# Performance work log

Hardware: AMD Instinct MI355X
Metric: run time of the kernel (lower is better)

The kernel has to match this reference:

```python
import jax, jax.numpy as jnp
import numpy as np

E = 8        # num_experts
TOPK = 2     # k
D = 1024     # input/output size
H = 4096     # expert hidden size


def setup_inputs() -> dict:
    key = jax.random.key(0)
    ks = jax.random.split(key, 8)
    s = 0.02
    return {
        "hidden_states": jax.random.normal(ks[0], (2, 2048, D), dtype=jnp.float32),
        "Wr": jax.random.normal(ks[1], (D, E), dtype=jnp.float32) * s,
        "br": jnp.zeros((E,), dtype=jnp.float32),
        "gate_bias": jnp.zeros((E,), dtype=jnp.float32),
        "W1": jax.random.normal(ks[2], (E, D, H), dtype=jnp.float32) * s,
        "b1": jnp.zeros((E, H), dtype=jnp.float32),
        "W2": jax.random.normal(ks[3], (E, H, D), dtype=jnp.float32) * s,
        "b2": jnp.zeros((E, D), dtype=jnp.float32),
    }


def reference(hidden_states, Wr, br, gate_bias, W1, b1, W2, b2):
    B, S, Din = hidden_states.shape
    x = hidden_states.reshape(B * S, Din)              # [T, D]
    # Router: logits + gate bias, top-k, softmax over the k selected logits
    logits = x @ Wr + br + gate_bias                   # [T, E]
    top_v, top_i = jax.lax.top_k(logits, TOPK)         # [T, k]
    probs = jax.nn.softmax(top_v, axis=-1)             # [T, k]
    # Scatter top-k probs into dense per-expert gate weights [T, E]
    gate = jnp.einsum("tk,tke->te", probs,
                      jax.nn.one_hot(top_i, E, dtype=probs.dtype))
    # Per-expert MLP (exact gelu, eval mode -> no dropout/noise),
    # weighted-combine; zero gate weight == token not routed to expert.
    out = jnp.zeros((B * S, W2.shape[-1]), dtype=x.dtype)
    for e in range(E):
        h = jax.nn.gelu(x @ W1[e] + b1[e], approximate=False)  # [T, H]
        y = h @ W2[e] + b2[e]                                  # [T, D]
        out = out + gate[:, e:e + 1] * y
    return out.reshape(B, S, -1)
```

## Files before the change

kernel.cpp:

```cpp
#include <hip/hip_runtime.h>
#include <hip/hip_bf16.h>
#include <stdint.h>
#include <stddef.h>


#define T_TOK 4096
#define DIM   1024
#define HID   4096
#define NE    8
#define MT_MAX 40

typedef unsigned short u16;
typedef __bf16 bf16x8 __attribute__((ext_vector_type(8)));
typedef float  f32x4  __attribute__((ext_vector_type(4)));
typedef u16    u16x8  __attribute__((ext_vector_type(8)));

__device__ __forceinline__ u16 f2bf(float f) {
  union { float f; uint32_t u; } v; v.f = f;
  uint32_t u = v.u;
  return (u16)((u + 0x7fffu + ((u >> 16) & 1u)) >> 16);
}

__device__ __forceinline__ void async_load16(const void* g, void* l) {
  typedef __attribute__((address_space(1))) void GPtr;
  typedef __attribute__((address_space(3))) void LPtr;
  __builtin_amdgcn_global_load_lds((GPtr*)g, (LPtr*)l, 16, 0, 0);
}

__global__ void router_kernel(const float* __restrict__ x, const float* __restrict__ Wr,
                              const float* __restrict__ br, const float* __restrict__ gb,
                              int* __restrict__ counts, int* __restrict__ lists,
                              float* __restrict__ gate_p) {
  const int t = blockIdx.x * 4 + (threadIdx.x >> 6);
  const int lane = threadIdx.x & 63;
  const float* xr = x + (size_t)t * DIM;
  float acc[NE];
#pragma unroll
  for (int e = 0; e < NE; ++e) acc[e] = 0.f;
#pragma unroll
  for (int i = 0; i < DIM / 64; ++i) {
    const int k = i * 64 + lane;
    const float xv = xr[k];
    const float4 w0 = *reinterpret_cast<const float4*>(Wr + (size_t)k * NE);
    const float4 w1 = *reinterpret_cast<const float4*>(Wr + (size_t)k * NE + 4);
    acc[0] += xv * w0.x; acc[1] += xv * w0.y; acc[2] += xv * w0.z; acc[3] += xv * w0.w;
    acc[4] += xv * w1.x; acc[5] += xv * w1.y; acc[6] += xv * w1.z; acc[7] += xv * w1.w;
  }
#pragma unroll
  for (int off = 32; off >= 1; off >>= 1) {
#pragma unroll
    for (int e = 0; e < NE; ++e) acc[e] += __shfl_xor(acc[e], off);
  }
  if (lane == 0) {
    float lg[NE];
#pragma unroll
    for (int e = 0; e < NE; ++e) lg[e] = acc[e] + br[e] + gb[e];
    int i0 = 0;
#pragma unroll
    for (int e = 1; e < NE; ++e) if (lg[e] > lg[i0]) i0 = e;
    int i1 = (i0 == 0) ? 1 : 0;
#pragma unroll
    for (int e = 0; e < NE; ++e) if (e != i0 && lg[e] > lg[i1]) i1 = e;
    const float ev = expf(lg[i1] - lg[i0]);
    const float p0 = 1.f / (1.f + ev);
    const float p1 = ev / (1.f + ev);
    const int pos0 = atomicAdd(&counts[i0], 1);
    lists[i0 * T_TOK + pos0] = t * 2 + 0;
    const int pos1 = atomicAdd(&counts[i1], 1);
    lists[i1 * T_TOK + pos1] = t * 2 + 1;
    gate_p[t * 2 + 0] = p0;
    gate_p[t * 2 + 1] = p1;
  }
}

__global__ void tile_table_kernel(const int* __restrict__ counts, int* __restrict__ tab) {
  if (threadIdx.x == 0) {
    int tot = 0;
    for (int e = 0; e < NE; ++e) {
      const int c = counts[e];
      const int nt = (c + 255) >> 8;
      for (int i = 0; i < nt && tot < MT_MAX; ++i) {
        tab[tot * 2] = e; tab[tot * 2 + 1] = i * 256; ++tot;
      }
    }
    for (; tot < MT_MAX; ++tot) tab[tot * 2] = -1;
  }
}

__global__ void cvt_x_kernel(const float* __restrict__ in, u16* __restrict__ out) {
  const int i = blockIdx.x * blockDim.x + threadIdx.x;
  const int t = i >> 7;
  const int d0 = (i & 127) * 8;
  const float4 a = *reinterpret_cast<const float4*>(in + (size_t)t * DIM + d0);
  const float4 b = *reinterpret_cast<const float4*>(in + (size_t)t * DIM + d0 + 4);
  u16x8 r;
  r[0] = f2bf(a.x); r[1] = f2bf(a.y); r[2] = f2bf(a.z); r[3] = f2bf(a.w);
  r[4] = f2bf(b.x); r[5] = f2bf(b.y); r[6] = f2bf(b.z); r[7] = f2bf(b.w);
  *reinterpret_cast<u16x8*>(out + (size_t)(d0 >> 6) * (T_TOK * 64) +
                            (size_t)t * 64 + (d0 & 63)) = r;
}

__global__ void cvt_w_kernel(const float* __restrict__ in, u16* __restrict__ out,
                             int K, int N) {
  __shared__ float tile[64][65];
  const int e = blockIdx.z;
  const int n0 = blockIdx.x * 64, k0 = blockIdx.y * 64;
  const int tid = threadIdx.x;
  const float* src = in + (size_t)e * K * N;
#pragma unroll
  for (int r = 0; r < 16; ++r) {
    const int kr = r * 4 + (tid >> 6);
    tile[kr][tid & 63] = src[(size_t)(k0 + kr) * N + n0 + (tid & 63)];
  }
  __syncthreads();
  u16* dst = out + (size_t)e * K * N + (size_t)(k0 >> 6) * ((size_t)N * 64);
#pragma unroll
  for (int r = 0; r < 8; ++r) {
    const int nr = r * 8 + (tid >> 5);
    const int kc = (tid & 31) * 2;
    ushort2 v;
    v.x = f2bf(tile[kc][nr]);
    v.y = f2bf(tile[kc + 1][nr]);
    *reinterpret_cast<ushort2*>(&dst[(size_t)(n0 + nr) * 64 + kc]) = v;
  }
}

template <int KT, int NT, int NSPLIT, int PHASE>
__global__ __launch_bounds__(512, 2)
void gemm_kernel(const u16* __restrict__ Abase, const u16* __restrict__ Bt,
                 const float* __restrict__ bias, const int* __restrict__ counts,
                 const int* __restrict__ lists, const float* __restrict__ gate_p,
                 const int* __restrict__ tab,
                 u16* __restrict__ hout, float* __restrict__ yout) {
  const int e = tab[blockIdx.x * 2];
  if (e < 0) return;
  const int m0 = tab[blockIdx.x * 2 + 1];
  const int cnt = counts[e];
  const int n0 = blockIdx.y * 256;
  const int z = blockIdx.z;
  const int kb64 = z * ((KT / NSPLIT) / 64);
  constexpr int nkt = (KT / NSPLIT) / 64;
  constexpr int niter = nkt / 2;
  constexpr size_t AKT = (PHASE == 1) ? (size_t)T_TOK * 64 : (size_t)T_TOK * 2 * 64;
  constexpr size_t BKT = (size_t)NT * 64;
  constexpr size_t HSLAB = (size_t)T_TOK * 2 * 64;

  const int tid = threadIdx.x;
  const int lane = tid & 63, w = tid >> 6;
  const int wm = w >> 2, wn = w & 3;
  const int bh = wn >> 1, bs = wn & 1;
  const int l15 = lane & 15, lks = lane >> 4;

  __shared__ alignas(16) u16 lds[65536];
  __shared__ int rowp[256];

  if (tid < 256) {
    const int idx = m0 + tid;
    rowp[tid] = lists[e * T_TOK + (idx < cnt ? idx : cnt - 1)];
  }
  __syncthreads();

  const int sslot = (tid & 7) ^ ((tid >> 3) & 7);
  const u16* aPtr[2][2];
  const u16* bPtr[2][2];
#pragma unroll
  for (int h = 0; h < 2; ++h)
#pragma unroll
    for (int s = 0; s < 2; ++s) {
      const int r = h * 128 + s * 64 + (tid >> 3);
      const int p = rowp[r];
      const int arow = (PHASE == 1) ? (p >> 1) : p;
      aPtr[h][s] = Abase + (size_t)kb64 * AKT + (size_t)arow * 64 + sslot * 8;
      bPtr[h][s] = Bt + (size_t)e * NT * KT + (size_t)kb64 * BKT +
                   (size_t)(n0 + r) * 64 + sslot * 8;
    }

  int aoff[2];
#pragma unroll
  for (int k = 0; k < 2; ++k)
    aoff[k] = l15 * 64 + (((k * 4 + lks) ^ (l15 & 7)) * 8);

  f32x4 acc[8][4];
#pragma unroll
  for (int a = 0; a < 8; ++a)
#pragma unroll
    for (int b = 0; b < 4; ++b) acc[a][b] = f32x4{0.f, 0.f, 0.f, 0.f};

  bf16x8 af[4][2], bfr[4][2];

#define RDA(C, FMH)                                                            \
  _Pragma("unroll") for (int f_ = 0; f_ < 4; ++f_)                             \
  _Pragma("unroll") for (int k_ = 0; k_ < 2; ++k_)                             \
    af[f_][k_] = *reinterpret_cast<const bf16x8*>(                             \
        &lds[(((C) * 2 + wm) * 2 + (FMH)) * 4096 + f_ * 1024 + aoff[k_]]);

#define RDB(C)                                                                 \
  _Pragma("unroll") for (int g_ = 0; g_ < 4; ++g_)                             \
  _Pragma("unroll") for (int k_ = 0; k_ < 2; ++k_)                             \
    bfr[g_][k_] = *reinterpret_cast<const bf16x8*>(                            \
        &lds[32768 + (((C) * 2 + bh) * 2 + bs) * 4096 + g_ * 1024 + aoff[k_]]);

#define SGA(C, S, TT)                                                          \
  _Pragma("unroll") for (int h_ = 0; h_ < 2; ++h_)                             \
    async_load16(aPtr[h_][S] + (size_t)(TT) * AKT,                             \
                 &lds[(((C) * 2 + h_) * 2 + (S)) * 4096 + w * 512]);

#define SGB(C, H, TT)                                                          \
  _Pragma("unroll") for (int s_ = 0; s_ < 2; ++s_)                             \
    async_load16(bPtr[H][s_] + (size_t)(TT) * BKT,                             \
                 &lds[32768 + (((C) * 2 + (H)) * 2 + s_) * 4096 + w * 512]);

#define MMQ(FMH, FNH)                                                          \
  _Pragma("unroll") for (int f_ = 0; f_ < 4; ++f_)                             \
  _Pragma("unroll") for (int g_ = 0; g_ < 2; ++g_)                             \
  _Pragma("unroll") for (int k_ = 0; k_ < 2; ++k_)                             \
    acc[(FMH) * 4 + f_][(FNH) * 2 + g_] =                                      \
        __builtin_amdgcn_mfma_f32_16x16x32_bf16(                               \
            af[f_][k_], bfr[(FNH) * 2 + g_][k_],                               \
            acc[(FMH) * 4 + f_][(FNH) * 2 + g_], 0, 0, 0);

#define CORE(FMH, FNH)                                                         \
  __builtin_amdgcn_s_barrier();                                                \
  asm volatile("s_waitcnt lgkmcnt(0)" ::: "memory");                           \
  __builtin_amdgcn_sched_barrier(0);                                           \
  __builtin_amdgcn_s_setprio(1);                                               \
  MMQ(FMH, FNH);                                                               \
  __builtin_amdgcn_s_setprio(0);                                               \
  __builtin_amdgcn_sched_barrier(0);

#define BAR() __builtin_amdgcn_s_barrier();

#define ITER(T, LAST)                                                          \
  {                                                                            \
    RDA(0, 0); RDB(0);                                                         \
    SGA(1, 1, (T) + 1);                                                        \
    CORE(0, 0) BAR()                                                           \
    if (!(LAST)) { SGA(0, 0, (T) + 2); }                                       \
    CORE(0, 1) BAR()                                                           \
    RDA(0, 1);                                                                 \
    if (!(LAST)) { SGB(0, 0, (T) + 2); }                                       \
    CORE(1, 0) BAR()                                                           \
    if (!(LAST)) { SGB(0, 1, (T) + 2); }                                       \
    CORE(1, 1)                                                                 \
    if (LAST) { asm volatile("s_waitcnt vmcnt(0)" ::: "memory"); }             \
    else      { asm volatile("s_waitcnt vmcnt(6)" ::: "memory"); }             \
    __builtin_amdgcn_sched_barrier(0);                                         \
    BAR()                                                                      \
    RDA(1, 0); RDB(1);                                                         \
    if (!(LAST)) { SGA(0, 1, (T) + 2); }                                       \
    CORE(0, 0) BAR()                                                           \
    if (!(LAST)) { SGA(1, 0, (T) + 3); }                                       \
    CORE(0, 1) BAR()                                                           \
    RDA(1, 1);                                                                 \
    if (!(LAST)) { SGB(1, 0, (T) + 3); }                                       \
    CORE(1, 0) BAR()                                                           \
    if (!(LAST)) { SGB(1, 1, (T) + 3); }                                       \
    CORE(1, 1)                                                                 \
    if (!(LAST)) {                                                             \
      asm volatile("s_waitcnt vmcnt(6)" ::: "memory");                         \
      __builtin_amdgcn_sched_barrier(0);                                       \
    }                                                                          \
    BAR()                                                                      \
  }

  SGA(0, 0, 0); SGB(0, 0, 0); SGB(0, 1, 0); SGA(0, 1, 0);
  SGA(1, 0, 1); SGB(1, 0, 1); SGB(1, 1, 1);
  asm volatile("s_waitcnt vmcnt(6)" ::: "memory");
  __builtin_amdgcn_sched_barrier(0);
  __builtin_amdgcn_s_barrier();

  for (int it = 0; it < niter - 1; ++it) {
    const int t = 2 * it;
    ITER(t, false);
  }
  ITER(nkt - 2, true);

#undef ITER
#undef CORE
#undef MMQ
#undef SGB
#undef SGA
#undef RDB
#undef RDA
#undef BAR

  const float* bias_e = bias + (size_t)e * NT;
  const float bz = (z == 0) ? 1.f : 0.f;
#pragma unroll
  for (int fm = 0; fm < 8; ++fm) {
    const int rbase = wm * 128 + (fm >> 2) * 64 + (fm & 3) * 16 + (lane >> 4) * 4;
#pragma unroll
    for (int r = 0; r < 4; ++r) {
      const int row = rbase + r;
      if (m0 + row >= cnt) continue;
      const int p = rowp[row];
#pragma unroll
      for (int nf = 0; nf < 4; ++nf) {
        const int n = n0 + wn * 64 + nf * 16 + l15;
        const float v = acc[fm][nf][r];
        if (PHASE == 1) {
          const float vb = v + bias_e[n];
          const float g = 0.5f * vb * (1.0f + erff(vb * 0.70710678118654752f));
          hout[(size_t)(n >> 6) * HSLAB + (size_t)p * 64 + (n & 63)] = f2bf(g);
        } else if (PHASE == 2) {
          yout[(size_t)z * T_TOK * 2 * NT + (size_t)p * NT + n] =
              gate_p[p] * (v + bz * bias_e[n]);
        } else {
          atomicAdd(&yout[(size_t)(p >> 1) * NT + n], gate_p[p] * (v + bz * bias_e[n]));
        }
      }
    }
  }
}

__global__ void combine4_kernel(const float* __restrict__ yp, float* __restrict__ out) {
  const int i = blockIdx.x * blockDim.x + threadIdx.x;
  const int t = i >> 8, d4 = i & 255;
  const size_t r0 = (size_t)(2 * t) * 256 + d4;
  const size_t zoff = (size_t)T_TOK * 2 * DIM / 4;
  const float4 a = reinterpret_cast<const float4*>(yp)[r0];
  const float4 b = reinterpret_cast<const float4*>(yp)[r0 + 256];
  const float4 c = reinterpret_cast<const float4*>(yp)[zoff + r0];
  const float4 d = reinterpret_cast<const float4*>(yp)[zoff + r0 + 256];
  float4 o;
  o.x = a.x + b.x + c.x + d.x; o.y = a.y + b.y + c.y + d.y;
  o.z = a.z + b.z + c.z + d.z; o.w = a.w + b.w + c.w + d.w;
  reinterpret_cast<float4*>(out)[i] = o;
}

extern "C" void kernel_launch(void* const* d_in, const int* in_sizes, int n_in,
                              void* d_out, int out_size, void* d_ws, size_t ws_size,
                              hipStream_t stream) {
  const float* x  = (const float*)d_in[0];
  const float* Wr = (const float*)d_in[1];
  const float* br = (const float*)d_in[2];
  const float* gb = (const float*)d_in[3];
  const float* W1 = (const float*)d_in[4];
  const float* b1 = (const float*)d_in[5];
  const float* W2 = (const float*)d_in[6];
  const float* b2 = (const float*)d_in[7];
  float* out = (float*)d_out;

  char* ws = (char*)d_ws;
  size_t off = 0;
  int*   counts = (int*)(ws + off);   off += 256;
  int*   ttab   = (int*)(ws + off);   off += 512;
  int*   lists  = (int*)(ws + off);   off += (size_t)NE * T_TOK * 4;
  float* gate_p = (float*)(ws + off); off += (size_t)T_TOK * 2 * 4;
  u16*   xb     = (u16*)(ws + off);   off += (size_t)T_TOK * DIM * 2;
  u16*   wbuf   = (u16*)(ws + off);   off += (size_t)NE * DIM * HID * 2;
  u16*   hbuf   = (u16*)(ws + off);   off += (size_t)T_TOK * 2 * HID * 2;
  float* ypair  = (float*)(ws + off);
  const size_t need_full = off + (size_t)2 * T_TOK * 2 * DIM * 4;
  const bool use_ypair = (ws_size >= need_full);

  hipMemsetAsync(counts, 0, 32, stream);
  router_kernel<<<T_TOK / 4, 256, 0, stream>>>(x, Wr, br, gb, counts, lists, gate_p);
  tile_table_kernel<<<1, 64, 0, stream>>>(counts, ttab);
  cvt_x_kernel<<<T_TOK * DIM / 8 / 256, 256, 0, stream>>>(x, xb);
  cvt_w_kernel<<<dim3(HID / 64, DIM / 64, NE), 256, 0, stream>>>(W1, wbuf, DIM, HID);
  gemm_kernel<DIM, HID, 1, 1><<<dim3(MT_MAX, HID / 256, 1), 512, 0, stream>>>(
      xb, wbuf, b1, counts, lists, gate_p, ttab, hbuf, nullptr);
  cvt_w_kernel<<<dim3(DIM / 64, HID / 64, NE), 256, 0, stream>>>(W2, wbuf, HID, DIM);
  if (use_ypair) {
    gemm_kernel<HID, DIM, 2, 2><<<dim3(MT_MAX, DIM / 256, 2), 512, 0, stream>>>(
        hbuf, wbuf, b2, counts, lists, gate_p, ttab, nullptr, ypair);
    combine4_kernel<<<T_TOK * DIM / 4 / 256, 256, 0, stream>>>(ypair, out);
  } else {
    hipMemsetAsync(out, 0, (size_t)out_size * 4, stream);
    gemm_kernel<HID, DIM, 2, 3><<<dim3(MT_MAX, DIM / 256, 2), 512, 0, stream>>>(
        hbuf, wbuf, b2, counts, lists, gate_p, ttab, nullptr, out);
  }
}
```

Before: 508.0 us.

## Replace quarter-tile ping-pong schedule with simple double-buffered K loop

Replaces the interleaved schedule in the GEMM main loop with a plain double-buffered loop. The old schedule split each K-tile into quarters, each behind its own barrier, and kept loads two tiles ahead. Now each step issues all A/B async loads for the next 64-wide K slice into the other buffer, computes two half-tiles of MFMAs, then waits for all loads and takes a single barrier. The LDS layout is simplified to contiguous 256-row buffers. The intent is to cut barrier and synchronisation overhead, at the cost of a shorter prefetch distance and a full vmcnt(0) wait each step that may expose memory latency.

Measured after the change: 498.6 us. No clear change (-1.9%).

```diff
diff --git a/kernel.cpp b/kernel.cpp
--- a/kernel.cpp
+++ b/kernel.cpp
@@ -140,7 +140,6 @@
   const int z = blockIdx.z;
   const int kb64 = z * ((KT / NSPLIT) / 64);
   constexpr int nkt = (KT / NSPLIT) / 64;
-  constexpr int niter = nkt / 2;
   constexpr size_t AKT = (PHASE == 1) ? (size_t)T_TOK * 64 : (size_t)T_TOK * 2 * 64;
   constexpr size_t BKT = (size_t)NT * 64;
   constexpr size_t HSLAB = (size_t)T_TOK * 2 * 64;
@@ -148,7 +147,6 @@
   const int tid = threadIdx.x;
   const int lane = tid & 63, w = tid >> 6;
   const int wm = w >> 2, wn = w & 3;
-  const int bh = wn >> 1, bs = wn & 1;
   const int l15 = lane & 15, lks = lane >> 4;
 
   __shared__ alignas(16) u16 lds[65536];
@@ -161,19 +159,17 @@
   __syncthreads();
 
   const int sslot = (tid & 7) ^ ((tid >> 3) & 7);
-  const u16* aPtr[2][2];
-  const u16* bPtr[2][2];
-#pragma unroll
-  for (int h = 0; h < 2; ++h)
-#pragma unroll
-    for (int s = 0; s < 2; ++s) {
-      const int r = h * 128 + s * 64 + (tid >> 3);
-      const int p = rowp[r];
-      const int arow = (PHASE == 1) ? (p >> 1) : p;
-      aPtr[h][s] = Abase + (size_t)kb64 * AKT + (size_t)arow * 64 + sslot * 8;
-      bPtr[h][s] = Bt + (size_t)e * NT * KT + (size_t)kb64 * BKT +
-                   (size_t)(n0 + r) * 64 + sslot * 8;
-    }
+  const u16* aP[4];
+  const u16* bP[4];
+#pragma unroll
+  for (int i = 0; i < 4; ++i) {
+    const int r = i * 64 + (tid >> 3);
+    const int p = rowp[r];
+    const int arow = (PHASE == 1) ? (p >> 1) : p;
+    aP[i] = Abase + (size_t)kb64 * AKT + (size_t)arow * 64 + sslot * 8;
+    bP[i] = Bt + (size_t)e * NT * KT + (size_t)kb64 * BKT +
+            (size_t)(n0 + r) * 64 + sslot * 8;
+  }
 
   int aoff[2];
 #pragma unroll
@@ -187,102 +183,70 @@
     for (int b = 0; b < 4; ++b) acc[a][b] = f32x4{0.f, 0.f, 0.f, 0.f};
 
   bf16x8 af[4][2], bfr[4][2];
+
+#define SGALL(C, TT)                                                           \
+  _Pragma("unroll") for (int i_ = 0; i_ < 4; ++i_)                             \
+    async_load16(aP[i_] + (size_t)(TT) * AKT,                                  \
+                 &lds[(C) * 16384 + (i_ * 64 + w * 8) * 64]);                  \
+  _Pragma("unroll") for (int i_ = 0; i_ < 4; ++i_)                             \
+    async_load16(bP[i_] + (size_t)(TT) * BKT,                                  \
+                 &lds[32768 + (C) * 16384 + (i_ * 64 + w * 8) * 64]);
 
 #define RDA(C, FMH)                                                            \
   _Pragma("unroll") for (int f_ = 0; f_ < 4; ++f_)                             \
   _Pragma("unroll") for (int k_ = 0; k_ < 2; ++k_)                             \
     af[f_][k_] = *reinterpret_cast<const bf16x8*>(                             \
-        &lds[(((C) * 2 + wm) * 2 + (FMH)) * 4096 + f_ * 1024 + aoff[k_]]);
+        &lds[(C) * 16384 + (wm * 128 + (FMH) * 64 + f_ * 16) * 64 + aoff[k_]]);
 
 #define RDB(C)                                                                 \
   _Pragma("unroll") for (int g_ = 0; g_ < 4; ++g_)                             \
   _Pragma("unroll") for (int k_ = 0; k_ < 2; ++k_)                             \
     bfr[g_][k_] = *reinterpret_cast<const bf16x8*>(                            \
-        &lds[32768 + (((C) * 2 + bh) * 2 + bs) * 4096 + g_ * 1024 + aoff[k_]]);
-
-#define SGA(C, S, TT)                                                          \
-  _Pragma("unroll") for (int h_ = 0; h_ < 2; ++h_)                             \
-    async_load16(aPtr[h_][S] + (size_t)(TT) * AKT,                             \
-                 &lds[(((C) * 2 + h_) * 2 + (S)) * 4096 + w * 512]);
-
-#define SGB(C, H, TT)                                                          \
-  _Pragma("unroll") for (int s_ = 0; s_ < 2; ++s_)                             \
-    async_load16(bPtr[H][s_] + (size_t)(TT) * BKT,                             \
-                 &lds[32768 + (((C) * 2 + (H)) * 2 + s_) * 4096 + w * 512]);
-
-#define MMQ(FMH, FNH)                                                          \
+        &lds[32768 + (C) * 16384 + (wn * 64 + g_ * 16) * 64 + aoff[k_]]);
+
+#define MMH(FMH)                                                               \
+  __builtin_amdgcn_s_setprio(1);                                               \
   _Pragma("unroll") for (int f_ = 0; f_ < 4; ++f_)                             \
-  _Pragma("unroll") for (int g_ = 0; g_ < 2; ++g_)                             \
+  _Pragma("unroll") for (int g_ = 0; g_ < 4; ++g_)                             \
   _Pragma("unroll") for (int k_ = 0; k_ < 2; ++k_)                             \
-    acc[(FMH) * 4 + f_][(FNH) * 2 + g_] =                                      \
-        __builtin_amdgcn_mfma_f32_16x16x32_bf16(                               \
-            af[f_][k_], bfr[(FNH) * 2 + g_][k_],                               \
-            acc[(FMH) * 4 + f_][(FNH) * 2 + g_], 0, 0, 0);
-
-#define CORE(FMH, FNH)                                                         \
-  __builtin_amdgcn_s_barrier();                                                \
-  asm volatile("s_waitcnt lgkmcnt(0)" ::: "memory");                           \
-  __builtin_amdgcn_sched_barrier(0);                                           \
-  __builtin_amdgcn_s_setprio(1);                                               \
-  MMQ(FMH, FNH);                                                               \
-  __builtin_amdgcn_s_setprio(0);                                               \
-  __builtin_amdgcn_sched_barrier(0);
-
-#define BAR() __builtin_amdgcn_s_barrier();
-
-#define ITER(T, LAST)                                                          \
+    acc[(FMH) * 4 + f_][g_] = __builtin_amdgcn_mfma_f32_16x16x32_bf16(         \
+        af[f_][k_], bfr[g_][k_], acc[(FMH) * 4 + f_][g_], 0, 0, 0);            \
+  __builtin_amdgcn_s_setprio(0);
+
+#define STEP(C, T, HASNEXT)                                                    \
   {                                                                            \
-    RDA(0, 0); RDB(0);                                                         \
-    SGA(1, 1, (T) + 1);                                                        \
-    CORE(0, 0) BAR()                                                           \
-    if (!(LAST)) { SGA(0, 0, (T) + 2); }                                       \
-    CORE(0, 1) BAR()                                                           \
-    RDA(0, 1);                                                                 \
-    if (!(LAST)) { SGB(0, 0, (T) + 2); }                                       \
-    CORE(1, 0) BAR()                                                           \
-    if (!(LAST)) { SGB(0, 1, (T) + 2); }                                       \
-    CORE(1, 1)                                                                 \
-    if (LAST) { asm volatile("s_waitcnt vmcnt(0)" ::: "memory"); }             \
-    else      { asm volatile("s_waitcnt vmcnt(6)" ::: "memory"); }             \
+    if (HASNEXT) { SGALL((C) ^ 1, (T) + 1); }                                  \
+    RDA(C, 0); RDB(C);                                                         \
+    asm volatile("s_waitcnt lgkmcnt(0)" ::: "memory");                         \
     __builtin_amdgcn_sched_barrier(0);                                         \
-    BAR()                                                                      \
-    RDA(1, 0); RDB(1);                                                         \
-    if (!(LAST)) { SGA(0, 1, (T) + 2); }                                       \
-    CORE(0, 0) BAR()                                                           \
-    if (!(LAST)) { SGA(1, 0, (T) + 3); }                                       \
-    CORE(0, 1) BAR()                                                           \
-    RDA(1, 1);                                                                 \
-    if (!(LAST)) { SGB(1, 0, (T) + 3); }                                       \
-    CORE(1, 0) BAR()                                                           \
-    if (!(LAST)) { SGB(1, 1, (T) + 3); }                                       \
-    CORE(1, 1)                                                                 \
-    if (!(LAST)) {                                                             \
-      asm volatile("s_waitcnt vmcnt(6)" ::: "memory");                         \
+    MMH(0);                                                                    \
+    RDA(C, 1);                                                                 \
+    asm volatile("s_waitcnt lgkmcnt(0)" ::: "memory");                         \
+    __builtin_amdgcn_sched_barrier(0);                                         \
+    MMH(1);                                                                    \
+    if (HASNEXT) {                                                             \
+      asm volatile("s_waitcnt vmcnt(0)" ::: "memory");                         \
       __builtin_amdgcn_sched_barrier(0);                                       \
+      __builtin_amdgcn_s_barrier();                                            \
     }                                                                          \
-    BAR()                                                                      \
-  }
-
-  SGA(0, 0, 0); SGB(0, 0, 0); SGB(0, 1, 0); SGA(0, 1, 0);
-  SGA(1, 0, 1); SGB(1, 0, 1); SGB(1, 1, 1);
-  asm volatile("s_waitcnt vmcnt(6)" ::: "memory");
+  }
+
+  SGALL(0, 0);
+  asm volatile("s_waitcnt vmcnt(0)" ::: "memory");
   __builtin_amdgcn_sched_barrier(0);
   __builtin_amdgcn_s_barrier();
 
-  for (int it = 0; it < niter - 1; ++it) {
-    const int t = 2 * it;
-    ITER(t, false);
-  }
-  ITER(nkt - 2, true);
-
-#undef ITER
-#undef CORE
-#undef MMQ
-#undef SGB
-#undef SGA
+#pragma unroll 1
+  for (int t = 0; t < nkt; t += 2) {
+    STEP(0, t, true);
+    STEP(1, t + 1, (t + 2 < nkt));
+  }
+
+#undef STEP
+#undef MMH
 #undef RDB
 #undef RDA
-#undef BAR
+#undef SGALL
 
   const float* bias_e = bias + (size_t)e * NT;
   const float bz = (z == 0) ? 1.f : 0.f;
```
